# Kernel optimization log

Hardware: AMD Instinct MI355X
Metric: run time of the kernel (lower is better)

The kernel has to match this reference:

```python
import jax, jax.numpy as jnp
import numpy as np

N = 32768
D_IN = 1728   # 192*3*3
D = 1024
C_CLS = 2


def setup_inputs() -> dict:
    key = jax.random.key(0)
    ks = jax.random.split(key, 8)
    # _initialize_weights: Linear weights ~ N(0, 0.01), biases zero
    x = jax.random.normal(ks[0], (N, D_IN), dtype=jnp.float32)
    w1 = jax.random.normal(ks[1], (D, D_IN), dtype=jnp.float32) * 0.01
    b1 = jnp.zeros((D,), jnp.float32)
    w2 = jax.random.normal(ks[2], (D, D), dtype=jnp.float32) * 0.01
    b2 = jnp.zeros((D,), jnp.float32)
    w_fc = jax.random.normal(ks[3], (C_CLS, D), dtype=jnp.float32) * 0.01
    b_fc = jnp.zeros((C_CLS,), jnp.float32)
    w_q = jax.random.normal(ks[4], (D, D), dtype=jnp.float32) * 0.01
    b_q = jnp.zeros((D,), jnp.float32)
    w_v = jax.random.normal(ks[5], (D, D), dtype=jnp.float32) * 0.01
    b_v = jnp.zeros((D,), jnp.float32)
    # Conv1d(2,2,kernel_size=1024): weight [out=2, in=2, k=1024]
    fan = C_CLS * D
    w_fcc = jax.random.uniform(ks[6], (C_CLS, C_CLS, D), jnp.float32,
                               -1.0 / np.sqrt(fan), 1.0 / np.sqrt(fan))
    b_fcc = jax.random.uniform(ks[7], (C_CLS,), jnp.float32,
                               -1.0 / np.sqrt(fan), 1.0 / np.sqrt(fan))
    return {"x": x, "w1": w1, "b1": b1, "w2": w2, "b2": b2,
            "w_fc": w_fc, "b_fc": b_fc, "w_q": w_q, "b_q": b_q,
            "w_v": w_v, "b_v": b_v, "w_fcc": w_fcc, "b_fcc": b_fcc}


def reference(x, w1, b1, w2, b2, w_fc, b_fc, w_q, b_q, w_v, b_v, w_fcc, b_fcc):
    # classifier MLP (dropout = identity in eval)
    h = jax.nn.relu(x @ w1.T + b1)          # [N, 1024]
    feat = jax.nn.relu(h @ w2.T + b2)       # [N, 1024]
    instance_pred = feat @ w_fc.T + b_fc    # [N, 2]
    V = feat @ w_v.T + b_v                  # [N, 1024]
    Q = feat @ w_q.T + b_q                  # [N, 1024]
    # torch.sort(..., descending=True)[1][0] == argmax per class column
    top_idx = jnp.argmax(instance_pred, axis=0)   # [2]
    m_feats = feat[top_idx]                 # [2, 1024]
    q_max = m_feats @ w_q.T + b_q           # [2, 1024]
    scale = jnp.sqrt(jnp.float32(Q.shape[1]))
    A = jax.nn.softmax((Q @ q_max.T) / scale, axis=0)  # softmax over instances, [N, 2]
    B = A.T @ V                             # [2, 1024]
    # Conv1d(2,2,k=1024) over length-1024 input -> single output position
    C = (jnp.einsum('oik,ik->o', w_fcc, B) + b_fcc).reshape(1, C_CLS)
    return instance_pred, C, A, B[None]
```

## Files before the change

kernel.cpp:

```cpp
#include <hip/hip_runtime.h>
#include <stdint.h>


typedef unsigned short u16;
typedef __attribute__((ext_vector_type(8))) short short8;
typedef __attribute__((ext_vector_type(4))) float floatx4;

#define TILE 128
#define BK 32

__device__ __forceinline__ float bf2f(u16 u) {
  union { unsigned u; float f; } x; x.u = ((unsigned)u) << 16; return x.f;
}
__device__ __forceinline__ u16 f2bf(float f) {
  union { float f; unsigned u; } x; x.f = f;
  return (u16)((x.u + 0x7fffu + ((x.u >> 16) & 1u)) >> 16);
}
__device__ __forceinline__ unsigned ordf(float f) {
  union { float f; unsigned u; } x; x.f = f;
  return (x.u & 0x80000000u) ? ~x.u : (x.u | 0x80000000u);
}
__device__ __forceinline__ void gload16(const void* g, void* l) {
  __builtin_amdgcn_global_load_lds(
      (const __attribute__((address_space(1))) void*)g,
      (__attribute__((address_space(3))) void*)l, 16, 0, 0);
}

template <int MODE>
__global__ __launch_bounds__(256) void gemm_bt(
    const u16* __restrict__ A, const u16* __restrict__ B,
    const float* __restrict__ bias, u16* __restrict__ O,
    float* __restrict__ OL, int K, int ntiles, int ldo) {
  __shared__ __align__(16) u16 As[TILE * BK];
  __shared__ __align__(16) u16 Bs[TILE * BK];

  const int nt = blockIdx.x % ntiles;
  const int mt = blockIdx.x / ntiles;
  const int m0 = mt * TILE, n0 = nt * TILE;
  const int tid = threadIdx.x;
  const int lane = tid & 63;
  const int wm = (tid >> 7) * 64;
  const int wn = ((tid >> 6) & 1) * 64;

  floatx4 acc[4][4];
#pragma unroll
  for (int i = 0; i < 4; ++i)
#pragma unroll
    for (int j = 0; j < 4; ++j) acc[i][j] = (floatx4){0.f, 0.f, 0.f, 0.f};

  const int srow = tid >> 2;
  const int scol = (tid & 3) * 8;
  const u16* Ag0 = A + (size_t)(m0 + srow) * K + scol;
  const u16* Ag1 = Ag0 + (size_t)64 * K;
  const u16* Bg0 = B + (size_t)(n0 + srow) * K + scol;
  const u16* Bg1 = Bg0 + (size_t)64 * K;
  u16* Al0 = As + tid * 8;
  u16* Al1 = Al0 + 256 * 8;
  u16* Bl0 = Bs + tid * 8;
  u16* Bl1 = Bl0 + 256 * 8;

  const u16* Af = As + (size_t)(wm + (lane & 15)) * BK + ((lane >> 4) * 8);
  const u16* Bf = Bs + (size_t)(wn + (lane & 15)) * BK + ((lane >> 4) * 8);

  const int kiters = K / BK;
  for (int kt = 0; kt < kiters; ++kt) {
    gload16(Ag0, Al0); gload16(Ag1, Al1);
    gload16(Bg0, Bl0); gload16(Bg1, Bl1);
    Ag0 += BK; Ag1 += BK; Bg0 += BK; Bg1 += BK;
    __syncthreads();
    short8 a[4], b[4];
#pragma unroll
    for (int f = 0; f < 4; ++f) {
      a[f] = *(const short8*)(Af + f * 16 * BK);
      b[f] = *(const short8*)(Bf + f * 16 * BK);
    }
#pragma unroll
    for (int i = 0; i < 4; ++i)
#pragma unroll
      for (int j = 0; j < 4; ++j)
        acc[i][j] = __builtin_amdgcn_mfma_f32_16x16x32_bf16(a[i], b[j],
                                                            acc[i][j], 0, 0, 0);
    __syncthreads();
  }

  const int er = (lane >> 4) * 4;
  const int ec = lane & 15;
  if (MODE == 0 || n0 < 1024) {
#pragma unroll
    for (int j = 0; j < 4; ++j) {
      const int col = n0 + wn + j * 16 + ec;
      const float bv = bias[col];
#pragma unroll
      for (int i = 0; i < 4; ++i) {
        const int row = m0 + wm + i * 16 + er;
#pragma unroll
        for (int r = 0; r < 4; ++r) {
          float v = acc[i][j][r] + bv;
          if (MODE == 0) v = fmaxf(v, 0.f);
          O[(size_t)(row + r) * ldo + col] = f2bf(v);
        }
      }
    }
  } else {
    if (wn == 0 && ec < 2) {
#pragma unroll
      for (int i = 0; i < 4; ++i) {
        const int row = m0 + wm + i * 16 + er;
#pragma unroll
        for (int r = 0; r < 4; ++r)
          OL[(size_t)(row + r) * 2 + ec] = acc[i][0][r];
      }
    }
  }
}

__global__ void k_init(u16* b3pad, float* Bbuf, unsigned long long* keys) {
  int i = blockIdx.x * 256 + threadIdx.x;
  if (i < 129024) b3pad[i] = 0;
  if (i < 2048) Bbuf[i] = 0.f;
  if (i < 2) keys[i] = 0ull;
}

__global__ void k_cast(const float* __restrict__ s, u16* __restrict__ d, int n4) {
  int i = blockIdx.x * 256 + threadIdx.x;
  if (i >= n4) return;
  float4 v = ((const float4*)s)[i];
  unsigned long long o = (unsigned long long)f2bf(v.x) |
                         ((unsigned long long)f2bf(v.y) << 16) |
                         ((unsigned long long)f2bf(v.z) << 32) |
                         ((unsigned long long)f2bf(v.w) << 48);
  ((unsigned long long*)d)[i] = o;
}

__global__ __launch_bounds__(256) void k_ip(const u16* __restrict__ feat,
                                            const float* __restrict__ wfc,
                                            const float* __restrict__ bfc,
                                            float* __restrict__ out_ip) {
  const int row = blockIdx.x * 4 + (threadIdx.x >> 6);
  const int lane = threadIdx.x & 63;
  const u16* fr = feat + (size_t)row * 1024 + lane * 16;
  const float* w0 = wfc + lane * 16;
  const float* w1 = wfc + 1024 + lane * 16;
  float s0 = 0.f, s1 = 0.f;
#pragma unroll
  for (int t = 0; t < 16; ++t) {
    float f = bf2f(fr[t]);
    s0 += f * w0[t];
    s1 += f * w1[t];
  }
#pragma unroll
  for (int off = 32; off > 0; off >>= 1) {
    s0 += __shfl_down(s0, off, 64);
    s1 += __shfl_down(s1, off, 64);
  }
  if (lane == 0) {
    out_ip[(size_t)row * 2 + 0] = s0 + bfc[0];
    out_ip[(size_t)row * 2 + 1] = s1 + bfc[1];
  }
}

__global__ __launch_bounds__(256) void k_argmax(const float* __restrict__ ip,
                                                unsigned long long* __restrict__ keys) {
  float m0 = -1e30f, m1 = -1e30f;
  int i0 = 0, i1 = 0;
  for (int i = blockIdx.x * 256 + threadIdx.x; i < 32768; i += 256 * 64) {
    float v0 = ip[2 * i], v1 = ip[2 * i + 1];
    if (v0 > m0) { m0 = v0; i0 = i; }
    if (v1 > m1) { m1 = v1; i1 = i; }
  }
  unsigned long long k0 =
      ((unsigned long long)ordf(m0) << 32) | (0xFFFFFFFFu - (unsigned)i0);
  unsigned long long k1 =
      ((unsigned long long)ordf(m1) << 32) | (0xFFFFFFFFu - (unsigned)i1);
#pragma unroll
  for (int off = 32; off > 0; off >>= 1) {
    unsigned long long t0 = __shfl_down(k0, off, 64);
    unsigned long long t1 = __shfl_down(k1, off, 64);
    if (t0 > k0) k0 = t0;
    if (t1 > k1) k1 = t1;
  }
  __shared__ unsigned long long s0[4], s1[4];
  const int lane = threadIdx.x & 63, wv = threadIdx.x >> 6;
  if (lane == 0) { s0[wv] = k0; s1[wv] = k1; }
  __syncthreads();
  if (threadIdx.x == 0) {
    for (int w = 1; w < 4; ++w) {
      if (s0[w] > k0) k0 = s0[w];
      if (s1[w] > k1) k1 = s1[w];
    }
    atomicMax(keys + 0, k0);
    atomicMax(keys + 1, k1);
  }
}

__global__ __launch_bounds__(256) void k_qmax(const u16* __restrict__ feat,
                                              const float* __restrict__ wq,
                                              const float* __restrict__ bq,
                                              const unsigned long long* __restrict__ keys,
                                              float* __restrict__ qmax) {
  const int gw = blockIdx.x * 4 + (threadIdx.x >> 6);
  const int c = gw >> 10, k = gw & 1023;
  const int lane = threadIdx.x & 63;
  const int idx = (int)(0xFFFFFFFFu - (unsigned)(keys[c] & 0xFFFFFFFFull));
  const u16* fr = feat + (size_t)idx * 1024 + lane * 16;
  const float* wr = wq + (size_t)k * 1024 + lane * 16;
  float s = 0.f;
#pragma unroll
  for (int t = 0; t < 16; ++t) s += bf2f(fr[t]) * wr[t];
#pragma unroll
  for (int off = 32; off > 0; off >>= 1) s += __shfl_down(s, off, 64);
  if (lane == 0) qmax[c * 1024 + k] = s + bq[k];
}

__global__ __launch_bounds__(256) void k_t(const float* __restrict__ wq,
                                           const float* __restrict__ qmax,
                                           u16* __restrict__ b3) {
  const int c = blockIdx.x >> 2;
  const int j = (blockIdx.x & 3) * 256 + threadIdx.x;
  float s = 0.f;
  for (int k = 0; k < 1024; ++k) s += qmax[c * 1024 + k] * wq[(size_t)k * 1024 + j];
  b3[(size_t)(1024 + c) * 1024 + j] = f2bf(s);
}

__global__ __launch_bounds__(256) void k_reduce(const float* __restrict__ lg,
                                                float* __restrict__ ms) {
  __shared__ float r0[256], r1[256];
  const int tid = threadIdx.x;
  float m0 = -1e30f, m1 = -1e30f;
  for (int i = tid; i < 32768; i += 256) {
    m0 = fmaxf(m0, lg[2 * i]);
    m1 = fmaxf(m1, lg[2 * i + 1]);
  }
  r0[tid] = m0; r1[tid] = m1;
  __syncthreads();
  for (int s = 128; s > 0; s >>= 1) {
    if (tid < s) {
      r0[tid] = fmaxf(r0[tid], r0[tid + s]);
      r1[tid] = fmaxf(r1[tid], r1[tid + s]);
    }
    __syncthreads();
  }
  m0 = r0[0]; m1 = r1[0];
  __syncthreads();
  float s0 = 0.f, s1 = 0.f;
  for (int i = tid; i < 32768; i += 256) {
    s0 += __expf((lg[2 * i] - m0) * 0.03125f);
    s1 += __expf((lg[2 * i + 1] - m1) * 0.03125f);
  }
  r0[tid] = s0; r1[tid] = s1;
  __syncthreads();
  for (int s = 128; s > 0; s >>= 1) {
    if (tid < s) { r0[tid] += r0[tid + s]; r1[tid] += r1[tid + s]; }
    __syncthreads();
  }
  if (tid == 0) { ms[0] = m0; ms[1] = m1; ms[2] = r0[0]; ms[3] = r1[0]; }
}

__global__ __launch_bounds__(256) void k_ab(const float* __restrict__ lg,
                                            const float* __restrict__ ms,
                                            const u16* __restrict__ V,
                                            float* __restrict__ outA,
                                            float* __restrict__ Bbuf) {
  const int tid = threadIdx.x;
  const int row0 = blockIdx.x * 256;
  const float m0 = ms[0], m1 = ms[1];
  const float inv0 = 1.f / ms[2], inv1 = 1.f / ms[3];
  {
    const int r = row0 + tid;
    outA[2 * r] = __expf((lg[2 * r] - m0) * 0.03125f) * inv0;
    outA[2 * r + 1] = __expf((lg[2 * r + 1] - m1) * 0.03125f) * inv1;
  }
  float p0[4] = {0, 0, 0, 0}, p1[4] = {0, 0, 0, 0};
  const int kb = tid * 4;
  for (int r = row0; r < row0 + 256; ++r) {
    const float a0 = __expf((lg[2 * r] - m0) * 0.03125f) * inv0;
    const float a1 = __expf((lg[2 * r + 1] - m1) * 0.03125f) * inv1;
    unsigned long long vv = *(const unsigned long long*)(V + (size_t)r * 1024 + kb);
    float f0 = bf2f((u16)vv), f1 = bf2f((u16)(vv >> 16));
    float f2 = bf2f((u16)(vv >> 32)), f3 = bf2f((u16)(vv >> 48));
    p0[0] += a0 * f0; p0[1] += a0 * f1; p0[2] += a0 * f2; p0[3] += a0 * f3;
    p1[0] += a1 * f0; p1[1] += a1 * f1; p1[2] += a1 * f2; p1[3] += a1 * f3;
  }
#pragma unroll
  for (int t = 0; t < 4; ++t) {
    atomicAdd(&Bbuf[kb + t], p0[t]);
    atomicAdd(&Bbuf[1024 + kb + t], p1[t]);
  }
}

__global__ __launch_bounds__(256) void k_c(const float* __restrict__ Bbuf,
                                           const float* __restrict__ wfcc,
                                           const float* __restrict__ bfcc,
                                           float* __restrict__ outC,
                                           float* __restrict__ outB) {
  __shared__ float r0[256], r1[256];
  const int tid = threadIdx.x;
  float s0 = 0.f, s1 = 0.f;
  for (int i = tid; i < 2048; i += 256) {
    float b = Bbuf[i];
    outB[i] = b;
    s0 += wfcc[i] * b;
    s1 += wfcc[2048 + i] * b;
  }
  r0[tid] = s0; r1[tid] = s1;
  __syncthreads();
  for (int s = 128; s > 0; s >>= 1) {
    if (tid < s) { r0[tid] += r0[tid + s]; r1[tid] += r1[tid + s]; }
    __syncthreads();
  }
  if (tid == 0) {
    outC[0] = r0[0] + bfcc[0];
    outC[1] = r1[0] + bfcc[1];
  }
}

extern "C" void kernel_launch(void* const* d_in, const int* in_sizes, int n_in,
                              void* d_out, int out_size, void* d_ws, size_t ws_size,
                              hipStream_t stream) {
  const float* x    = (const float*)d_in[0];
  const float* w1   = (const float*)d_in[1];
  const float* b1   = (const float*)d_in[2];
  const float* w2   = (const float*)d_in[3];
  const float* b2   = (const float*)d_in[4];
  const float* wfc  = (const float*)d_in[5];
  const float* bfc  = (const float*)d_in[6];
  const float* wq   = (const float*)d_in[7];
  const float* bq   = (const float*)d_in[8];
  const float* wv   = (const float*)d_in[9];
  const float* bv   = (const float*)d_in[10];
  const float* wfcc = (const float*)d_in[11];
  const float* bfcc = (const float*)d_in[12];

  float* out   = (float*)d_out;
  float* outIP = out;
  float* outC  = out + 65536;
  float* outA  = out + 65538;
  float* outB  = out + 131074;

  char* ws = (char*)d_ws;
  u16* XB  = (u16*)(ws);
  u16* HB  = (u16*)(ws + 113246208);
  u16* FB  = (u16*)(ws + 180355072);
  u16* W1B = (u16*)(ws + 247463936);
  u16* W2B = (u16*)(ws + 251002880);
  u16* B3  = (u16*)(ws + 253100032);
  float* LG = (float*)(ws + 255459328);
  float* QM = (float*)(ws + 255721472);
  unsigned long long* KEYS = (unsigned long long*)(ws + 255729664);
  float* MS   = (float*)(ws + 255729680);
  float* BBUF = (float*)(ws + 255729696);

  k_init<<<504, 256, 0, stream>>>(B3 + 1026 * 1024, BBUF, KEYS);
  k_cast<<<55296, 256, 0, stream>>>(x, XB, 56623104 / 4);
  k_cast<<<1728, 256, 0, stream>>>(w1, W1B, 1769472 / 4);
  k_cast<<<1024, 256, 0, stream>>>(w2, W2B, 1048576 / 4);
  k_cast<<<1024, 256, 0, stream>>>(wv, B3, 1048576 / 4);

  gemm_bt<0><<<256 * 8, 256, 0, stream>>>(XB, W1B, b1, HB, nullptr, 1728, 8, 1024);
  gemm_bt<0><<<256 * 8, 256, 0, stream>>>(HB, W2B, b2, FB, nullptr, 1024, 8, 1024);

  k_ip<<<8192, 256, 0, stream>>>(FB, wfc, bfc, outIP);
  k_argmax<<<64, 256, 0, stream>>>(outIP, KEYS);
  k_qmax<<<512, 256, 0, stream>>>(FB, wq, bq, KEYS, QM);
  k_t<<<8, 256, 0, stream>>>(wq, QM, B3);

  gemm_bt<1><<<256 * 9, 256, 0, stream>>>(FB, B3, bv, HB, LG, 1024, 9, 1024);

  k_reduce<<<1, 256, 0, stream>>>(LG, MS);
  k_ab<<<128, 256, 0, stream>>>(LG, MS, HB, outA, BBUF);
  k_c<<<1, 256, 0, stream>>>(BBUF, wfcc, bfcc, outC, outB);
}
```

Baseline: 921.8 us.

## Swizzle GEMM LDS layout, remap blocks per XCD, parallelize small reductions

The GEMM now maps blocks so that each XCD works on a contiguous range of M tiles, which should improve L2 reuse of the A rows. It also XOR-style rotates the 16-byte chunk placement in LDS to cut bank conflicts on fragment reads. The q_max-times-Wq transpose product is split over 32 blocks with partial sums and a separate cast kernel, and k_ab uses 256 blocks of 128 rows instead of 128 blocks of 256 rows. Together these raise parallelism in the small serial kernels, at the cost of one extra launch and more atomics.

```diff
diff --git a/kernel.cpp b/kernel.cpp
--- a/kernel.cpp
+++ b/kernel.cpp
@@ -34,8 +34,11 @@
   __shared__ __align__(16) u16 As[TILE * BK];
   __shared__ __align__(16) u16 Bs[TILE * BK];
 
-  const int nt = blockIdx.x % ntiles;
-  const int mt = blockIdx.x / ntiles;
+  const int xcd = blockIdx.x & 7;
+  const int j = blockIdx.x >> 3;
+  const int mstride = gridDim.x / (ntiles << 3);
+  const int mt = xcd * mstride + j / ntiles;
+  const int nt = j % ntiles;
   const int m0 = mt * TILE, n0 = nt * TILE;
   const int tid = threadIdx.x;
   const int lane = tid & 63;
@@ -46,21 +49,23 @@
 #pragma unroll
   for (int i = 0; i < 4; ++i)
 #pragma unroll
-    for (int j = 0; j < 4; ++j) acc[i][j] = (floatx4){0.f, 0.f, 0.f, 0.f};
+    for (int jf = 0; jf < 4; ++jf) acc[i][jf] = (floatx4){0.f, 0.f, 0.f, 0.f};
 
   const int srow = tid >> 2;
-  const int scol = (tid & 3) * 8;
-  const u16* Ag0 = A + (size_t)(m0 + srow) * K + scol;
+  const int sq = ((tid & 3) - srow) & 3;
+  const u16* Ag0 = A + (size_t)(m0 + srow) * K + sq * 8;
   const u16* Ag1 = Ag0 + (size_t)64 * K;
-  const u16* Bg0 = B + (size_t)(n0 + srow) * K + scol;
+  const u16* Bg0 = B + (size_t)(n0 + srow) * K + sq * 8;
   const u16* Bg1 = Bg0 + (size_t)64 * K;
   u16* Al0 = As + tid * 8;
   u16* Al1 = Al0 + 256 * 8;
   u16* Bl0 = Bs + tid * 8;
   u16* Bl1 = Bl0 + 256 * 8;
 
-  const u16* Af = As + (size_t)(wm + (lane & 15)) * BK + ((lane >> 4) * 8);
-  const u16* Bf = Bs + (size_t)(wn + (lane & 15)) * BK + ((lane >> 4) * 8);
+  const int fr = lane & 15;
+  const int fq = lane >> 4;
+  const u16* Af = As + (size_t)(wm + fr) * BK + (((fq + fr) & 3) * 8);
+  const u16* Bf = Bs + (size_t)(wn + fr) * BK + (((fq + fr) & 3) * 8);
 
   const int kiters = K / BK;
   for (int kt = 0; kt < kiters; ++kt) {
@@ -77,9 +82,9 @@
 #pragma unroll
     for (int i = 0; i < 4; ++i)
 #pragma unroll
-      for (int j = 0; j < 4; ++j)
-        acc[i][j] = __builtin_amdgcn_mfma_f32_16x16x32_bf16(a[i], b[j],
-                                                            acc[i][j], 0, 0, 0);
+      for (int jf = 0; jf < 4; ++jf)
+        acc[i][jf] = __builtin_amdgcn_mfma_f32_16x16x32_bf16(a[i], b[jf],
+                                                             acc[i][jf], 0, 0, 0);
     __syncthreads();
   }
 
@@ -87,15 +92,15 @@
   const int ec = lane & 15;
   if (MODE == 0 || n0 < 1024) {
 #pragma unroll
-    for (int j = 0; j < 4; ++j) {
-      const int col = n0 + wn + j * 16 + ec;
+    for (int jf = 0; jf < 4; ++jf) {
+      const int col = n0 + wn + jf * 16 + ec;
       const float bv = bias[col];
 #pragma unroll
       for (int i = 0; i < 4; ++i) {
         const int row = m0 + wm + i * 16 + er;
 #pragma unroll
         for (int r = 0; r < 4; ++r) {
-          float v = acc[i][j][r] + bv;
+          float v = acc[i][jf][r] + bv;
           if (MODE == 0) v = fmaxf(v, 0.f);
           O[(size_t)(row + r) * ldo + col] = f2bf(v);
         }
@@ -214,12 +219,26 @@
 
 __global__ __launch_bounds__(256) void k_t(const float* __restrict__ wq,
                                            const float* __restrict__ qmax,
-                                           u16* __restrict__ b3) {
-  const int c = blockIdx.x >> 2;
-  const int j = (blockIdx.x & 3) * 256 + threadIdx.x;
+                                           float* __restrict__ tpart) {
+  const int jb = blockIdx.x & 3, kp = blockIdx.x >> 2;
+  const int jcol = jb * 256 + threadIdx.x;
+  float s0 = 0.f, s1 = 0.f;
+  for (int k = kp * 128; k < kp * 128 + 128; ++k) {
+    float w = wq[(size_t)k * 1024 + jcol];
+    s0 += qmax[k] * w;
+    s1 += qmax[1024 + k] * w;
+  }
+  tpart[kp * 2048 + jcol] = s0;
+  tpart[kp * 2048 + 1024 + jcol] = s1;
+}
+
+__global__ __launch_bounds__(256) void k_tcast(const float* __restrict__ tpart,
+                                               u16* __restrict__ b3) {
+  const int i = blockIdx.x * 256 + threadIdx.x;
   float s = 0.f;
-  for (int k = 0; k < 1024; ++k) s += qmax[c * 1024 + k] * wq[(size_t)k * 1024 + j];
-  b3[(size_t)(1024 + c) * 1024 + j] = f2bf(s);
+#pragma unroll
+  for (int kp = 0; kp < 8; ++kp) s += tpart[kp * 2048 + i];
+  b3[(size_t)(1024 + (i >> 10)) * 1024 + (i & 1023)] = f2bf(s);
 }
 
 __global__ __launch_bounds__(256) void k_reduce(const float* __restrict__ lg,
@@ -262,17 +281,18 @@
                                             float* __restrict__ outA,
                                             float* __restrict__ Bbuf) {
   const int tid = threadIdx.x;
-  const int row0 = blockIdx.x * 256;
+  const int row0 = blockIdx.x * 128;
   const float m0 = ms[0], m1 = ms[1];
   const float inv0 = 1.f / ms[2], inv1 = 1.f / ms[3];
   {
-    const int r = row0 + tid;
-    outA[2 * r] = __expf((lg[2 * r] - m0) * 0.03125f) * inv0;
-    outA[2 * r + 1] = __expf((lg[2 * r + 1] - m1) * 0.03125f) * inv1;
+    const int r = row0 + (tid >> 1);
+    const int c = tid & 1;
+    outA[2 * r + c] =
+        __expf((lg[2 * r + c] - (c ? m1 : m0)) * 0.03125f) * (c ? inv1 : inv0);
   }
   float p0[4] = {0, 0, 0, 0}, p1[4] = {0, 0, 0, 0};
   const int kb = tid * 4;
-  for (int r = row0; r < row0 + 256; ++r) {
+  for (int r = row0; r < row0 + 128; ++r) {
     const float a0 = __expf((lg[2 * r] - m0) * 0.03125f) * inv0;
     const float a1 = __expf((lg[2 * r + 1] - m1) * 0.03125f) * inv1;
     unsigned long long vv = *(const unsigned long long*)(V + (size_t)r * 1024 + kb);
@@ -342,6 +362,7 @@
   u16* HB  = (u16*)(ws + 113246208);
   u16* FB  = (u16*)(ws + 180355072);
   u16* W1B = (u16*)(ws + 247463936);
+  float* TPART = (float*)(ws + 247463936);
   u16* W2B = (u16*)(ws + 251002880);
   u16* B3  = (u16*)(ws + 253100032);
   float* LG = (float*)(ws + 255459328);
@@ -362,11 +383,12 @@
   k_ip<<<8192, 256, 0, stream>>>(FB, wfc, bfc, outIP);
   k_argmax<<<64, 256, 0, stream>>>(outIP, KEYS);
   k_qmax<<<512, 256, 0, stream>>>(FB, wq, bq, KEYS, QM);
-  k_t<<<8, 256, 0, stream>>>(wq, QM, B3);
+  k_t<<<32, 256, 0, stream>>>(wq, QM, TPART);
+  k_tcast<<<8, 256, 0, stream>>>(TPART, B3);
 
   gemm_bt<1><<<256 * 9, 256, 0, stream>>>(FB, B3, bv, HB, LG, 1024, 9, 1024);
 
   k_reduce<<<1, 256, 0, stream>>>(LG, MS);
-  k_ab<<<128, 256, 0, stream>>>(LG, MS, HB, outA, BBUF);
+  k_ab<<<256, 256, 0, stream>>>(LG, MS, HB, outA, BBUF);
   k_c<<<1, 256, 0, stream>>>(BBUF, wfcc, bfcc, outC, outB);
 }
```

Measured after the change: 854.3 us. 1.08x faster.
